# Performance work log

Hardware: AMD Instinct MI355X
Metric: run time of the kernel (lower is better)

The kernel has to match this reference:

```python
import jax, jax.numpy as jnp
import numpy as np

KS = 3      # kernel size
PAD = 1     # zero padding
STRIDE = 1
N = KS * KS # 9 sampling points per pixel


def _deform_conv(feature, offset, weight):
    """DeformConv2d: bilinear sample at learned offsets then 3x3 conv (no bias)."""
    b, c, h, w = feature.shape
    x = jnp.pad(feature, ((0, 0), (0, 0), (PAD, PAD), (PAD, PAD)))
    hp, wp = h + 2 * PAD, w + 2 * PAD
    dt = feature.dtype
    # p_n: kernel grid offsets, x(rows) first then y(cols) -> (2N,)
    rng = jnp.arange(-(KS - 1) // 2, (KS - 1) // 2 + 1, dtype=dt)
    pn_x, pn_y = jnp.meshgrid(rng, rng, indexing='ij')
    # p_0: base sampling grid starting at 1 (accounts for zero padding)
    p0_x, p0_y = jnp.meshgrid(jnp.arange(1, h + 1, dtype=dt),
                              jnp.arange(1, w + 1, dtype=dt), indexing='ij')
    # sampling locations p = p_0 + p_n + offset, split into x/y -> (b,h,w,N)
    off = jnp.transpose(offset, (0, 2, 3, 1))  # (b,h,w,2N)
    px = p0_x[None, :, :, None] + pn_x.reshape(-1)[None, None, None, :] + off[..., :N]
    py = p0_y[None, :, :, None] + pn_y.reshape(-1)[None, None, None, :] + off[..., N:]
    q_lt_x = jnp.clip(jnp.floor(px), 0, hp - 1)
    q_lt_y = jnp.clip(jnp.floor(py), 0, wp - 1)
    q_rb_x = jnp.clip(jnp.floor(px) + 1, 0, hp - 1)
    q_rb_y = jnp.clip(jnp.floor(py) + 1, 0, wp - 1)
    px = jnp.clip(px, 0, hp - 1)
    py = jnp.clip(py, 0, wp - 1)
    # bilinear weights for the 4 corners
    g_lt = (1 + (q_lt_x - px)) * (1 + (q_lt_y - py))
    g_rb = (1 - (q_rb_x - px)) * (1 - (q_rb_y - py))
    g_lb = (1 + (q_lt_x - px)) * (1 - (q_rb_y - py))
    g_rt = (1 - (q_rb_x - px)) * (1 + (q_lt_y - py))
    x_flat = x.reshape(b, c, hp * wp)

    def gather(qx, qy):
        idx = (qx * wp + qy).astype(jnp.int32).reshape(b, 1, -1)
        v = jnp.take_along_axis(x_flat, jnp.broadcast_to(idx, (b, c, h * w * N)), axis=2)
        return v.reshape(b, c, h, w, N)

    x_off = (g_lt[:, None] * gather(q_lt_x, q_lt_y)
             + g_rb[:, None] * gather(q_rb_x, q_rb_y)
             + g_lb[:, None] * gather(q_lt_x, q_rb_y)
             + g_rt[:, None] * gather(q_rb_x, q_lt_y))  # (b,c,h,w,N)
    # equivalent of _reshape_x_offset + conv(ks, stride=ks)
    x_off = x_off.reshape(b, c, h, w, KS, KS)
    return jnp.einsum('bchwij,ocij->bohw', x_off, weight)


def setup_inputs() -> dict:
    key = jax.random.key(0)
    k1, k2, k3 = jax.random.split(key, 3)
    B, C, H, W = 4, 256, 64, 64
    feature = jax.random.normal(k1, (B, C, H, W), dtype=jnp.float32)
    offset = jax.random.normal(k2, (B, 2 * N, H, W), dtype=jnp.float32)
    weight = jax.random.normal(k3, (C, C, KS, KS), dtype=jnp.float32) / np.sqrt(C * N)
    return {"feature": feature, "offset": offset, "weight": weight}


def reference(feature, offset, weight):
    f1 = jax.nn.relu(_deform_conv(feature, offset, weight))
    return jax.nn.relu(f1 + feature)
```

## Files before the change

kernel.cpp:

```cpp
#include <hip/hip_runtime.h>
#include <hip/hip_bf16.h>

#define HW    4096
#define J_TOT 16384
#define K_TOT 2304
#define C_CH  256

typedef unsigned short u16;
typedef unsigned int   u32;
typedef __attribute__((ext_vector_type(8))) short short8;
typedef __attribute__((ext_vector_type(4))) float f32x4;
typedef __attribute__((ext_vector_type(8))) unsigned short us8;
typedef __attribute__((ext_vector_type(4))) unsigned short us4;

__device__ __forceinline__ float b2f(u16 u) { return __uint_as_float(((u32)u) << 16); }
__device__ __forceinline__ u16 f2b(float x) {
  u32 u = __float_as_uint(x);
  u += 0x7FFFu + ((u >> 16) & 1u);
  return (u16)(u >> 16);
}
__device__ __forceinline__ float blo(u32 u) { return __uint_as_float(u << 16); }
__device__ __forceinline__ float bhi(u32 u) { return __uint_as_float(u & 0xFFFF0000u); }

__device__ __forceinline__ us8 interp8(us8 r0, us8 r1, us8 r2, us8 r3,
                                       float g0, float g1, float g2, float g3) {
  us8 o;
  const u32* p0 = (const u32*)&r0;
  const u32* p1 = (const u32*)&r1;
  const u32* p2 = (const u32*)&r2;
  const u32* p3 = (const u32*)&r3;
  u32* po = (u32*)&o;
#pragma unroll
  for (int i = 0; i < 4; i++) {
    u32 a = p0[i], b = p1[i], c = p2[i], d = p3[i];
    float2 v;
    v.x = g0 * blo(a) + g1 * blo(b) + g2 * blo(c) + g3 * blo(d);
    v.y = g0 * bhi(a) + g1 * bhi(b) + g2 * bhi(c) + g3 * bhi(d);
    __hip_bfloat162 pk = __float22bfloat162_rn(v);
    po[i] = *reinterpret_cast<u32*>(&pk);
  }
  return o;
}

__device__ __forceinline__ int detect_bf16(const u16* f, int t, int nthr, int* cnt) {
  if (t == 0) *cnt = 0;
  __syncthreads();
  int hits = 0;
  for (int i = t; i < 2048; i += nthr) {
    u16 u = f[2 * i];
    int e = (u >> 7) & 0xFF;
    hits += (e >= 100 && e <= 141) ? 1 : 0;
  }
  atomicAdd(cnt, hits);
  __syncthreads();
  return (*cnt > 1024) ? 1 : 0;
}

__global__ __launch_bounds__(256) void k_prep(const void* __restrict__ featv,
                                              const void* __restrict__ wv,
                                              u16* __restrict__ ftr,
                                              u16* __restrict__ Wr) {
  __shared__ int cnt;
  __shared__ u16 tile[32][33];
  int t = threadIdx.x;
  int isbf = detect_bf16((const u16*)featv, t, 256, &cnt);
  int bi = blockIdx.x;
  if (bi < 4096) {
    int b = bi >> 10;
    int y = (bi >> 7) & 7;
    int x = bi & 127;
    int hw0 = x << 5;
    int c0 = y << 5;
    int tx = t & 31, ty = t >> 5;
    if (isbf) {
      const u16* f = (const u16*)featv;
#pragma unroll
      for (int i = 0; i < 4; i++) {
        int c = c0 + ty + i * 8;
        tile[ty + i * 8][tx] = f[(((size_t)(b * C_CH + c)) << 12) + hw0 + tx];
      }
    } else {
      const float* f = (const float*)featv;
#pragma unroll
      for (int i = 0; i < 4; i++) {
        int c = c0 + ty + i * 8;
        tile[ty + i * 8][tx] = f2b(f[(((size_t)(b * C_CH + c)) << 12) + hw0 + tx]);
      }
    }
    __syncthreads();
#pragma unroll
    for (int i = 0; i < 4; i++) {
      int hw = hw0 + ty + i * 8;
      ftr[(((size_t)(b * HW + hw)) << 8) + c0 + tx] = tile[tx][ty + i * 8];
    }
  } else {
    int idx = (bi - 4096) * 256 + t;
    int c = idx & 255;
    int n = (idx >> 8) % 9;
    int o = idx / K_TOT;
    int src = (o * 256 + c) * 9 + n;
    if (isbf) Wr[idx] = ((const u16*)wv)[src];
    else      Wr[idx] = f2b(((const float*)wv)[src]);
  }
}

__global__ __launch_bounds__(512) void k_fused(const u16* __restrict__ Wr,
                                               const u16* __restrict__ ftr,
                                               const void* __restrict__ offv,
                                               const void* __restrict__ featv,
                                               void* __restrict__ outv) {
  __shared__ u16 Bs[2][64 * 256];
  __shared__ u16 cq[9][64][4];
  __shared__ float cg[9][64][4];
  __shared__ int cnt;
  int t = threadIdx.x;
  int isbf = detect_bf16((const u16*)featv, t, 512, &cnt);

  int jb = blockIdx.x << 6;
  int b  = jb >> 12;
  int hw0 = jb & (HW - 1);
  int wave = t >> 6, lane = t & 63;
  int lr = lane & 15, lk = lane >> 4;
  int lane16 = t & 15, grp16 = t >> 4;

  for (int task = t; task < 576; task += 512) {
    int px = task & 63, n = task >> 6;
    int phw = hw0 + px;
    int ph = phw >> 6, pw = phw & 63;
    size_t obi = (((size_t)(b * 18 + n)) << 12) + phw;
    float ox, oy;
    if (isbf) {
      const u16* po = (const u16*)offv;
      ox = b2f(po[obi]);
      oy = b2f(po[obi + (9u << 12)]);
    } else {
      const float* po = (const float*)offv;
      ox = po[obi];
      oy = po[obi + (9u << 12)];
    }
    int ki = n / 3, kj = n % 3;
    float sx = (float)(ph + ki) + ox;
    float sy = (float)(pw + kj) + oy;
    float fx = floorf(sx), fy = floorf(sy);
    float qltx = fminf(fmaxf(fx, 0.f), 65.f);
    float qlty = fminf(fmaxf(fy, 0.f), 65.f);
    float qrbx = fminf(fmaxf(fx + 1.f, 0.f), 65.f);
    float qrby = fminf(fmaxf(fy + 1.f, 0.f), 65.f);
    float pcx = fminf(fmaxf(sx, 0.f), 65.f);
    float pcy = fminf(fmaxf(sy, 0.f), 65.f);
    float dltx = 1.f + (qltx - pcx);
    float drbx = 1.f - (qrbx - pcx);
    float dlty = 1.f + (qlty - pcy);
    float drby = 1.f - (qrby - pcy);
    float g0 = dltx * dlty;
    float g1 = drbx * drby;
    float g2 = dltx * drby;
    float g3 = drbx * dlty;
    int x0 = (int)qltx, y0 = (int)qlty, x1 = (int)qrbx, y1 = (int)qrby;
    int v0 = (x0 >= 1 && x0 <= 64 && y0 >= 1 && y0 <= 64);
    int v1 = (x1 >= 1 && x1 <= 64 && y1 >= 1 && y1 <= 64);
    int v2 = (x0 >= 1 && x0 <= 64 && y1 >= 1 && y1 <= 64);
    int v3 = (x1 >= 1 && x1 <= 64 && y0 >= 1 && y0 <= 64);
    cq[n][px][0] = v0 ? (u16)(((x0 - 1) << 6) + (y0 - 1)) : (u16)0;
    cq[n][px][1] = v1 ? (u16)(((x1 - 1) << 6) + (y1 - 1)) : (u16)0;
    cq[n][px][2] = v2 ? (u16)(((x0 - 1) << 6) + (y1 - 1)) : (u16)0;
    cq[n][px][3] = v3 ? (u16)(((x1 - 1) << 6) + (y0 - 1)) : (u16)0;
    cg[n][px][0] = v0 ? g0 : 0.f;
    cg[n][px][1] = v1 ? g1 : 0.f;
    cg[n][px][2] = v2 ? g2 : 0.f;
    cg[n][px][3] = v3 ? g3 : 0.f;
  }

  f32x4 acc[2][4];
  f32x4 zero = {0.f, 0.f, 0.f, 0.f};
#pragma unroll
  for (int i = 0; i < 2; i++)
#pragma unroll
    for (int j = 0; j < 4; j++) acc[i][j] = zero;

  const u16* awp[2];
  awp[0] = Wr + (size_t)(wave * 32 + lr) * K_TOT + lk * 8;
  awp[1] = awp[0] + (size_t)16 * K_TOT;

  int bbase = b << 12;

  us8 P[2][4];

  auto loadGroup = [&](int n1, int g) {
#pragma unroll
    for (int u = 0; u < 2; u++) {
      int px = grp16 + g * 32;
      int c16 = u * 16 + lane16;
      int ch = c16 * 8;
      us4 q = *(const us4*)&cq[n1][px][0];
      P[u][0] = *(const us8*)(ftr + ((bbase + q.x) << 8) + ch);
      P[u][1] = *(const us8*)(ftr + ((bbase + q.y) << 8) + ch);
      P[u][2] = *(const us8*)(ftr + ((bbase + q.z) << 8) + ch);
      P[u][3] = *(const us8*)(ftr + ((bbase + q.w) << 8) + ch);
    }
  };
  auto interpGroup = [&](int n1, int g, u16* dstp) {
#pragma unroll
    for (int u = 0; u < 2; u++) {
      int px = grp16 + g * 32;
      int c16 = u * 16 + lane16;
      float4 g4 = *(const float4*)&cg[n1][px][0];
      us8 ov = interp8(P[u][0], P[u][1], P[u][2], P[u][3], g4.x, g4.y, g4.z, g4.w);
      int cs = c16 ^ (px & 7);
      *(us8*)(&Bs[(n1) & 1][px * 256 + cs * 8]) = ov;
      (void)dstp;
    }
  };
  auto consume4 = [&](int n, int kc0) {
    const u16* srcp = Bs[n & 1];
#pragma unroll
    for (int k2 = 0; k2 < 4; k2++) {
      int kc = kc0 + k2;
      short8 Af[2], Bf[4];
#pragma unroll
      for (int oi = 0; oi < 2; oi++)
        Af[oi] = *(const short8*)(awp[oi] + (n << 8) + kc * 32);
#pragma unroll
      for (int ji = 0; ji < 4; ji++) {
        int row = ji * 16 + lr;
        int cs = (kc * 4 + lk) ^ (row & 7);
        Bf[ji] = *(const short8*)(&srcp[row * 256 + cs * 8]);
      }
#pragma unroll
      for (int oi = 0; oi < 2; oi++)
#pragma unroll
        for (int ji = 0; ji < 4; ji++)
          acc[oi][ji] = __builtin_amdgcn_mfma_f32_16x16x32_bf16(Af[oi], Bf[ji], acc[oi][ji], 0, 0, 0);
    }
  };

  __syncthreads();

  loadGroup(0, 0); interpGroup(0, 0, nullptr);
  loadGroup(0, 1); interpGroup(0, 1, nullptr);
  __syncthreads();

  for (int n = 0; n < 9; n++) {
    if (n < 8) loadGroup(n + 1, 0);
    consume4(n, 0);
    if (n < 8) { interpGroup(n + 1, 0, nullptr); loadGroup(n + 1, 1); }
    consume4(n, 4);
    if (n < 8) interpGroup(n + 1, 1, nullptr);
    __syncthreads();
  }

#pragma unroll
  for (int oi = 0; oi < 2; oi++) {
#pragma unroll
    for (int ji = 0; ji < 4; ji++) {
      int j = jb + ji * 16 + lr;
      int hww = j & (HW - 1);
      int o0 = wave * 32 + oi * 16 + lk * 4;
#pragma unroll
      for (int r = 0; r < 4; r++) {
        size_t oidx = (((size_t)(b * C_CH + o0 + r)) << 12) + hww;
        float v = acc[oi][ji][r];
        v = fmaxf(v, 0.f);
        float ft = isbf ? b2f(((const u16*)featv)[oidx]) : ((const float*)featv)[oidx];
        v = fmaxf(v + ft, 0.f);
        if (isbf) ((u16*)outv)[oidx] = f2b(v);
        else      ((float*)outv)[oidx] = v;
      }
    }
  }
}

extern "C" void kernel_launch(void* const* d_in, const int* in_sizes, int n_in,
                              void* d_out, int out_size, void* d_ws, size_t ws_size,
                              hipStream_t stream) {
  const void* feat = d_in[0];
  const void* offs = d_in[1];
  const void* wght = d_in[2];

  const size_t off_wr   = 0;
  const size_t off_ftr  = off_wr + (size_t)1179648;
  const size_t need     = off_ftr + (size_t)8388608;
  if (ws_size < need) return;

  char* ws = (char*)d_ws;
  u16* Wr   = (u16*)(ws + off_wr);
  u16* ftr  = (u16*)(ws + off_ftr);

  k_prep<<<4096 + 2304, 256, 0, stream>>>(feat, wght, ftr, Wr);
  k_fused<<<J_TOT / 64, 512, 0, stream>>>(Wr, ftr, offs, feat, d_out);
}
```

Baseline: 155.2 us.

## Shrink fused block to 32 pixels with 4 waves each covering 64 outputs

Changes the fused deformable-conv GEMM tile from 64 pixels × 256 outputs over 8 waves to 32 pixels × 256 outputs over 4 waves. Each wave now owns 64 output channels and 32 pixels, so the per-wave MFMA tile becomes 4×2 instead of 2×4. The grid doubles to 512 blocks and shared memory per block halves, which should fill more CUs and allow more resident blocks. In exchange, each weight fragment is reused across fewer pixels, so total weight reads from global/L2 double, and the gather/interp work per thread is unchanged.

```diff
diff --git a/kernel.cpp b/kernel.cpp
--- a/kernel.cpp
+++ b/kernel.cpp
@@ -5,6 +5,7 @@
 #define J_TOT 16384
 #define K_TOT 2304
 #define C_CH  256
+#define PX    32
 
 typedef unsigned short u16;
 typedef unsigned int   u32;
@@ -104,27 +105,27 @@
   }
 }
 
-__global__ __launch_bounds__(512) void k_fused(const u16* __restrict__ Wr,
+__global__ __launch_bounds__(256) void k_fused(const u16* __restrict__ Wr,
                                                const u16* __restrict__ ftr,
                                                const void* __restrict__ offv,
                                                const void* __restrict__ featv,
                                                void* __restrict__ outv) {
-  __shared__ u16 Bs[2][64 * 256];
-  __shared__ u16 cq[9][64][4];
-  __shared__ float cg[9][64][4];
+  __shared__ u16 Bs[2][PX * 256];
+  __shared__ u16 cq[9][PX][4];
+  __shared__ float cg[9][PX][4];
   __shared__ int cnt;
   int t = threadIdx.x;
-  int isbf = detect_bf16((const u16*)featv, t, 512, &cnt);
-
-  int jb = blockIdx.x << 6;
+  int isbf = detect_bf16((const u16*)featv, t, 256, &cnt);
+
+  int jb = blockIdx.x * PX;
   int b  = jb >> 12;
   int hw0 = jb & (HW - 1);
   int wave = t >> 6, lane = t & 63;
   int lr = lane & 15, lk = lane >> 4;
   int lane16 = t & 15, grp16 = t >> 4;
 
-  for (int task = t; task < 576; task += 512) {
-    int px = task & 63, n = task >> 6;
+  for (int task = t; task < 9 * PX; task += 256) {
+    int px = task & (PX - 1), n = task / PX;
     int phw = hw0 + px;
     int ph = phw >> 6, pw = phw & 63;
     size_t obi = (((size_t)(b * 18 + n)) << 12) + phw;
@@ -171,44 +172,43 @@
     cg[n][px][3] = v3 ? g3 : 0.f;
   }
 
-  f32x4 acc[2][4];
+  f32x4 acc[4][2];
   f32x4 zero = {0.f, 0.f, 0.f, 0.f};
 #pragma unroll
-  for (int i = 0; i < 2; i++)
-#pragma unroll
-    for (int j = 0; j < 4; j++) acc[i][j] = zero;
-
-  const u16* awp[2];
-  awp[0] = Wr + (size_t)(wave * 32 + lr) * K_TOT + lk * 8;
-  awp[1] = awp[0] + (size_t)16 * K_TOT;
+  for (int i = 0; i < 4; i++)
+#pragma unroll
+    for (int j = 0; j < 2; j++) acc[i][j] = zero;
+
+  const u16* awp[4];
+#pragma unroll
+  for (int oi = 0; oi < 4; oi++)
+    awp[oi] = Wr + (size_t)(wave * 64 + oi * 16 + lr) * K_TOT + lk * 8;
 
   int bbase = b << 12;
 
   us8 P[2][4];
 
-  auto loadGroup = [&](int n1, int g) {
+  auto loadGroup = [&](int n1, int s) {
+    int px = grp16 + s * 16;
+    us4 q = *(const us4*)&cq[n1][px][0];
 #pragma unroll
     for (int u = 0; u < 2; u++) {
-      int px = grp16 + g * 32;
-      int c16 = u * 16 + lane16;
-      int ch = c16 * 8;
-      us4 q = *(const us4*)&cq[n1][px][0];
+      int ch = (u * 16 + lane16) * 8;
       P[u][0] = *(const us8*)(ftr + ((bbase + q.x) << 8) + ch);
       P[u][1] = *(const us8*)(ftr + ((bbase + q.y) << 8) + ch);
       P[u][2] = *(const us8*)(ftr + ((bbase + q.z) << 8) + ch);
       P[u][3] = *(const us8*)(ftr + ((bbase + q.w) << 8) + ch);
     }
   };
-  auto interpGroup = [&](int n1, int g, u16* dstp) {
+  auto interpGroup = [&](int n1, int s) {
+    int px = grp16 + s * 16;
+    float4 g4 = *(const float4*)&cg[n1][px][0];
 #pragma unroll
     for (int u = 0; u < 2; u++) {
-      int px = grp16 + g * 32;
       int c16 = u * 16 + lane16;
-      float4 g4 = *(const float4*)&cg[n1][px][0];
       us8 ov = interp8(P[u][0], P[u][1], P[u][2], P[u][3], g4.x, g4.y, g4.z, g4.w);
       int cs = c16 ^ (px & 7);
-      *(us8*)(&Bs[(n1) & 1][px * 256 + cs * 8]) = ov;
-      (void)dstp;
+      *(us8*)(&Bs[n1 & 1][px * 256 + cs * 8]) = ov;
     }
   };
   auto consume4 = [&](int n, int kc0) {
@@ -216,46 +216,46 @@
 #pragma unroll
     for (int k2 = 0; k2 < 4; k2++) {
       int kc = kc0 + k2;
-      short8 Af[2], Bf[4];
-#pragma unroll
-      for (int oi = 0; oi < 2; oi++)
+      short8 Af[4], Bf[2];
+#pragma unroll
+      for (int oi = 0; oi < 4; oi++)
         Af[oi] = *(const short8*)(awp[oi] + (n << 8) + kc * 32);
 #pragma unroll
-      for (int ji = 0; ji < 4; ji++) {
+      for (int ji = 0; ji < 2; ji++) {
         int row = ji * 16 + lr;
         int cs = (kc * 4 + lk) ^ (row & 7);
         Bf[ji] = *(const short8*)(&srcp[row * 256 + cs * 8]);
       }
 #pragma unroll
-      for (int oi = 0; oi < 2; oi++)
-#pragma unroll
-        for (int ji = 0; ji < 4; ji++)
+      for (int oi = 0; oi < 4; oi++)
+#pragma unroll
+        for (int ji = 0; ji < 2; ji++)
           acc[oi][ji] = __builtin_amdgcn_mfma_f32_16x16x32_bf16(Af[oi], Bf[ji], acc[oi][ji], 0, 0, 0);
     }
   };
 
   __syncthreads();
 
-  loadGroup(0, 0); interpGroup(0, 0, nullptr);
-  loadGroup(0, 1); interpGroup(0, 1, nullptr);
+  loadGroup(0, 0); interpGroup(0, 0);
+  loadGroup(0, 1); interpGroup(0, 1);
   __syncthreads();
 
   for (int n = 0; n < 9; n++) {
     if (n < 8) loadGroup(n + 1, 0);
     consume4(n, 0);
-    if (n < 8) { interpGroup(n + 1, 0, nullptr); loadGroup(n + 1, 1); }
+    if (n < 8) { interpGroup(n + 1, 0); loadGroup(n + 1, 1); }
     consume4(n, 4);
-    if (n < 8) interpGroup(n + 1, 1, nullptr);
+    if (n < 8) interpGroup(n + 1, 1);
     __syncthreads();
   }
 
 #pragma unroll
-  for (int oi = 0; oi < 2; oi++) {
-#pragma unroll
-    for (int ji = 0; ji < 4; ji++) {
+  for (int oi = 0; oi < 4; oi++) {
+#pragma unroll
+    for (int ji = 0; ji < 2; ji++) {
       int j = jb + ji * 16 + lr;
       int hww = j & (HW - 1);
-      int o0 = wave * 32 + oi * 16 + lk * 4;
+      int o0 = wave * 64 + oi * 16 + lk * 4;
 #pragma unroll
       for (int r = 0; r < 4; r++) {
         size_t oidx = (((size_t)(b * C_CH + o0 + r)) << 12) + hww;
@@ -287,5 +287,5 @@
   u16* ftr  = (u16*)(ws + off_ftr);
 
   k_prep<<<4096 + 2304, 256, 0, stream>>>(feat, wght, ftr, Wr);
-  k_fused<<<J_TOT / 64, 512, 0, stream>>>(Wr, ftr, offs, feat, d_out);
-}
+  k_fused<<<J_TOT / PX, 256, 0, stream>>>(Wr, ftr, offs, feat, d_out);
+}
```

Result: slower. 181.5 us (+17.0%).
